# Performance work log

Measured on AMD Instinct MI355X. Metric: run time of the kernel, lower is better.

The kernel has to match this reference:

```python
import jax, jax.numpy as jnp
import numpy as np

B, T, OUT, H = 4096, 128, 64, 200


def lstm_cell(x_t, h, c, Wih, Whh, b):
    # PyTorch gate order: input, forget, cell(g), output
    gates = x_t @ Wih.T + h @ Whh.T + b  # [B, 4H]
    i, f, g, o = jnp.split(gates, 4, axis=-1)
    c = jax.nn.sigmoid(f) * c + jax.nn.sigmoid(i) * jnp.tanh(g)
    h = jax.nn.sigmoid(o) * jnp.tanh(c)
    return h, c


def lstm_layer(xs, Wih, Whh, b, h0, c0):
    # xs: [T, B, D] -> ys: [T, B, H], final (h, c)
    def step(carry, x_t):
        h, c = lstm_cell(x_t, carry[0], carry[1], Wih, Whh, b)
        return (h, c), h
    (h, c), ys = jax.lax.scan(step, (h0, c0), xs)
    return ys, h, c


def setup_inputs() -> dict:
    key = jax.random.key(0)
    ks = jax.random.split(key, 16)
    s = 0.05
    inp = {"x": jax.random.normal(ks[0], (B, T), dtype=jnp.float32)}
    # encoder layer 0 (input size 1), layer 1 (input size H)
    inp["enc_Wih0"] = jax.random.normal(ks[1], (4 * H, 1), jnp.float32) * s
    inp["enc_Whh0"] = jax.random.normal(ks[2], (4 * H, H), jnp.float32) * s
    inp["enc_b0"] = jnp.zeros((4 * H,), jnp.float32)
    inp["enc_Wih1"] = jax.random.normal(ks[3], (4 * H, H), jnp.float32) * s
    inp["enc_Whh1"] = jax.random.normal(ks[4], (4 * H, H), jnp.float32) * s
    inp["enc_b1"] = jnp.zeros((4 * H,), jnp.float32)
    # decoder layers
    inp["dec_Wih0"] = jax.random.normal(ks[5], (4 * H, 1), jnp.float32) * s
    inp["dec_Whh0"] = jax.random.normal(ks[6], (4 * H, H), jnp.float32) * s
    inp["dec_b0"] = jnp.zeros((4 * H,), jnp.float32)
    inp["dec_Wih1"] = jax.random.normal(ks[7], (4 * H, H), jnp.float32) * s
    inp["dec_Whh1"] = jax.random.normal(ks[8], (4 * H, H), jnp.float32) * s
    inp["dec_b1"] = jnp.zeros((4 * H,), jnp.float32)
    # output linear: hid -> 1
    inp["lin_W"] = jax.random.normal(ks[9], (1, H), jnp.float32) * s
    inp["lin_b"] = jnp.zeros((1,), jnp.float32)
    return inp


def reference(x, enc_Wih0, enc_Whh0, enc_b0, enc_Wih1, enc_Whh1, enc_b1,
              dec_Wih0, dec_Whh0, dec_b0, dec_Wih1, dec_Whh1, dec_b1,
              lin_W, lin_b):
    b = x.shape[0]
    z = jnp.zeros((b, H), x.dtype)
    xs = x.T[:, :, None]  # [T, B, 1]
    # encoder (2-layer LSTM; dropout is a no-op in eval mode)
    ys1, h1, c1 = lstm_layer(xs, enc_Wih0, enc_Whh0, enc_b0, z, z)
    _, h2, c2 = lstm_layer(ys1, enc_Wih1, enc_Whh1, enc_b1, z, z)

    def dec_step(carry, _):
        h1, c1, h2, c2, inp = carry
        h1, c1 = lstm_cell(inp, h1, c1, dec_Wih0, dec_Whh0, dec_b0)
        h2, c2 = lstm_cell(h1, h2, c2, dec_Wih1, dec_Whh1, dec_b1)
        pred = h2 @ lin_W.T + lin_b  # [B, 1]
        return (h1, c1, h2, c2, pred), pred[:, 0]

    carry0 = (h1, c1, h2, c2, x[:, -1:])
    _, preds = jax.lax.scan(dec_step, carry0, None, length=OUT)  # [OUT, B]
    return preds.T  # [B, OUT]
```

## Files before the change

### kernel.cpp

```cpp
#include <hip/hip_runtime.h>
#include <math.h>

#define HID   200
#define G4    800
#define BB    16
#define NTH   512
#define SEQT  128
#define NOUT  64
#define WKP   224
#define AST   232
#define GST   802
#define MATU  (G4 * WKP)

typedef __attribute__((ext_vector_type(8))) short short8;
typedef __attribute__((ext_vector_type(4))) float f32x4;
typedef unsigned short ushort_t;

__device__ __forceinline__ unsigned short bf16_rne(float v) {
    unsigned int u = __float_as_uint(v);
    u = u + 0x7FFFu + ((u >> 16) & 1u);
    return (unsigned short)(u >> 16);
}

__global__ void prep_weights(const float* __restrict__ s0, const float* __restrict__ s1,
                             const float* __restrict__ s2, const float* __restrict__ s3,
                             const float* __restrict__ s4, const float* __restrict__ s5,
                             unsigned short* __restrict__ ws) {
    const float* src;
    int m = blockIdx.y;
    switch (m) {
        case 0: src = s0; break;
        case 1: src = s1; break;
        case 2: src = s2; break;
        case 3: src = s3; break;
        case 4: src = s4; break;
        default: src = s5; break;
    }
    int i = blockIdx.x * blockDim.x + threadIdx.x;
    int n = i / WKP;
    int k = i - n * WKP;
    float v = (k < HID) ? src[n * HID + k] : 0.0f;
    unsigned short hi = bf16_rne(v);
    float rem = v - __uint_as_float(((unsigned int)hi) << 16);
    unsigned short lo = bf16_rne(rem);
    ws[(size_t)(2 * m) * MATU + i]     = hi;
    ws[(size_t)(2 * m + 1) * MATU + i] = lo;
}

__device__ __forceinline__ short8 ldA(const unsigned short* h, int lane, int c) {
    return *(const short8*)(h + (lane & 15) * AST + c * 32 + ((lane >> 4) << 3));
}

template<int NT>
__device__ __forceinline__ void mm_pass(const unsigned short* __restrict__ Whi,
                                        const unsigned short* __restrict__ Wlo,
                                        const unsigned short* hhi, const unsigned short* hlo,
                                        int lane, int tile0, f32x4* acc) {
    short8 ahi[7], alo[7];
#pragma unroll
    for (int c = 0; c < 7; ++c) { ahi[c] = ldA(hhi, lane, c); alo[c] = ldA(hlo, lane, c); }
    const int ko   = (lane >> 4) << 3;
    const int nrow = lane & 15;
#pragma unroll
    for (int t = 0; t < NT; ++t) {
        const unsigned short* wp = Whi + (size_t)((tile0 + t) * 16 + nrow) * WKP + ko;
        const unsigned short* wq = Wlo + (size_t)((tile0 + t) * 16 + nrow) * WKP + ko;
#pragma unroll
        for (int c = 0; c < 7; ++c) {
            short8 bhi = *(const short8*)(wp + c * 32);
            short8 blo = *(const short8*)(wq + c * 32);
            acc[t] = __builtin_amdgcn_mfma_f32_16x16x32_bf16(ahi[c], bhi, acc[t], 0, 0, 0);
            acc[t] = __builtin_amdgcn_mfma_f32_16x16x32_bf16(ahi[c], blo, acc[t], 0, 0, 0);
            acc[t] = __builtin_amdgcn_mfma_f32_16x16x32_bf16(alo[c], bhi, acc[t], 0, 0, 0);
        }
    }
}

template<int NT>
__device__ __forceinline__ void cell_mm_s(float* gates,
        const unsigned short* Whi, const unsigned short* Wlo,
        const unsigned short* hhi, const unsigned short* hlo,
        const float* __restrict__ bias, const float* __restrict__ wih,
        const float* xcol, int lane, int tile0) {
    f32x4 acc[NT];
    const int nrow = lane & 15;
    const int bg   = (lane >> 4) << 2;
#pragma unroll
    for (int t = 0; t < NT; ++t) {
        int n = (tile0 + t) * 16 + nrow;
        float bj = bias[n], wj = wih[n];
#pragma unroll
        for (int r = 0; r < 4; ++r) acc[t][r] = fmaf(xcol[bg + r], wj, bj);
    }
    mm_pass<NT>(Whi, Wlo, hhi, hlo, lane, tile0, acc);
#pragma unroll
    for (int t = 0; t < NT; ++t) {
        int n = (tile0 + t) * 16 + nrow;
#pragma unroll
        for (int r = 0; r < 4; ++r) gates[(bg + r) * GST + n] = acc[t][r];
    }
}

template<int NT>
__device__ __forceinline__ void cell_mm_v(float* gates,
        const unsigned short* Wihhi, const unsigned short* Wihlo,
        const unsigned short* Whhhi, const unsigned short* Whhlo,
        const unsigned short* hxhi, const unsigned short* hxlo,
        const unsigned short* hhhi, const unsigned short* hhlo,
        const float* __restrict__ bias, int lane, int tile0) {
    f32x4 acc[NT];
    const int nrow = lane & 15;
    const int bg   = (lane >> 4) << 2;
#pragma unroll
    for (int t = 0; t < NT; ++t) {
        float bj = bias[(tile0 + t) * 16 + nrow];
        acc[t] = (f32x4){bj, bj, bj, bj};
    }
    mm_pass<NT>(Wihhi, Wihlo, hxhi, hxlo, lane, tile0, acc);
    mm_pass<NT>(Whhhi, Whhlo, hhhi, hhlo, lane, tile0, acc);
#pragma unroll
    for (int t = 0; t < NT; ++t) {
        int n = (tile0 + t) * 16 + nrow;
#pragma unroll
        for (int r = 0; r < 4; ++r) gates[(bg + r) * GST + n] = acc[t][r];
    }
}

__device__ __forceinline__ float fsig(float v) {
    return __builtin_amdgcn_rcpf(1.0f + __expf(-v));
}
__device__ __forceinline__ float ftanh(float v) {
    return 1.0f - 2.0f * __builtin_amdgcn_rcpf(__expf(2.0f * v) + 1.0f);
}

__device__ __forceinline__ void cell_ew(const float* gates,
                                        unsigned short* hhi, unsigned short* hlo,
                                        float* cv, int tid) {
#pragma unroll
    for (int r = 0; r < 7; ++r) {
        int i = tid + r * NTH;
        if (i < BB * HID) {
            int b = i / HID;
            int m = i - b * HID;
            const float* g = gates + b * GST;
            float gi = g[m], gf = g[HID + m], gg = g[2 * HID + m], go = g[3 * HID + m];
            float cp = cv[r];
            float cn = fsig(gf) * cp + fsig(gi) * ftanh(gg);
            cv[r] = cn;
            float h = fsig(go) * ftanh(cn);
            unsigned short hb = bf16_rne(h);
            float rem = h - __uint_as_float(((unsigned int)hb) << 16);
            unsigned short lb = bf16_rne(rem);
            hhi[b * AST + m] = hb;
            hlo[b * AST + m] = lb;
        }
    }
}

__global__ __launch_bounds__(NTH, 2)
void lstm_mfma(const float* __restrict__ x,
               const float* __restrict__ eWih0, const float* __restrict__ eB0,
               const float* __restrict__ eB1,
               const float* __restrict__ dWih0, const float* __restrict__ dB0,
               const float* __restrict__ dB1,
               const float* __restrict__ linW, const float* __restrict__ linb,
               const unsigned short* __restrict__ wst,
               float* __restrict__ out) {
    extern __shared__ char smraw[];
    float* gates = (float*)smraw;
    float* xsT   = gates + BB * GST;
    float* linWs = xsT + SEQT * BB;
    float* predb = linWs + HID;
    float* part  = predb + BB;
    unsigned short* h1hi = (unsigned short*)(part + BB * 4);
    unsigned short* h1lo = h1hi + BB * AST;
    unsigned short* h2hi = h1lo + BB * AST;
    unsigned short* h2lo = h2hi + BB * AST;

    const unsigned short* eWhh0hi = wst;
    const unsigned short* eWhh0lo = wst + MATU;
    const unsigned short* eWih1hi = wst + 2 * MATU;
    const unsigned short* eWih1lo = wst + 3 * MATU;
    const unsigned short* eWhh1hi = wst + 4 * MATU;
    const unsigned short* eWhh1lo = wst + 5 * MATU;
    const unsigned short* dWhh0hi = wst + 6 * MATU;
    const unsigned short* dWhh0lo = wst + 7 * MATU;
    const unsigned short* dWih1hi = wst + 8 * MATU;
    const unsigned short* dWih1lo = wst + 9 * MATU;
    const unsigned short* dWhh1hi = wst + 10 * MATU;
    const unsigned short* dWhh1lo = wst + 11 * MATU;

    const int tid  = threadIdx.x;
    const int lane = tid & 63;
    const int w    = tid >> 6;
    const int b0g  = blockIdx.x * BB;
    const int tile0 = (w < 2) ? 7 * w : 14 + 6 * (w - 2);

    for (int i = tid; i < BB * AST; i += NTH) {
        h1hi[i] = 0; h1lo[i] = 0; h2hi[i] = 0; h2lo[i] = 0;
    }
    for (int i = tid; i < BB * SEQT; i += NTH) {
        int b = i >> 7, t = i & (SEQT - 1);
        xsT[t * BB + b] = x[(size_t)(b0g + b) * SEQT + t];
    }
    for (int i = tid; i < HID; i += NTH) linWs[i] = linW[i];
    float c1v[7], c2v[7];
#pragma unroll
    for (int r = 0; r < 7; ++r) { c1v[r] = 0.0f; c2v[r] = 0.0f; }
    __syncthreads();

    for (int t = 0; t < SEQT; ++t) {
        const float* xcol = xsT + t * BB;
        if (w < 2) cell_mm_s<7>(gates, eWhh0hi, eWhh0lo, h1hi, h1lo, eB0, eWih0, xcol, lane, tile0);
        else       cell_mm_s<6>(gates, eWhh0hi, eWhh0lo, h1hi, h1lo, eB0, eWih0, xcol, lane, tile0);
        __syncthreads();
        cell_ew(gates, h1hi, h1lo, c1v, tid);
        __syncthreads();
        if (w < 2) cell_mm_v<7>(gates, eWih1hi, eWih1lo, eWhh1hi, eWhh1lo, h1hi, h1lo, h2hi, h2lo, eB1, lane, tile0);
        else       cell_mm_v<6>(gates, eWih1hi, eWih1lo, eWhh1hi, eWhh1lo, h1hi, h1lo, h2hi, h2lo, eB1, lane, tile0);
        __syncthreads();
        cell_ew(gates, h2hi, h2lo, c2v, tid);
        __syncthreads();
    }

    if (tid < BB) predb[tid] = xsT[(SEQT - 1) * BB + tid];
    __syncthreads();

    for (int s = 0; s < NOUT; ++s) {
        if (w < 2) cell_mm_s<7>(gates, dWhh0hi, dWhh0lo, h1hi, h1lo, dB0, dWih0, predb, lane, tile0);
        else       cell_mm_s<6>(gates, dWhh0hi, dWhh0lo, h1hi, h1lo, dB0, dWih0, predb, lane, tile0);
        __syncthreads();
        cell_ew(gates, h1hi, h1lo, c1v, tid);
        __syncthreads();
        if (w < 2) cell_mm_v<7>(gates, dWih1hi, dWih1lo, dWhh1hi, dWhh1lo, h1hi, h1lo, h2hi, h2lo, dB1, lane, tile0);
        else       cell_mm_v<6>(gates, dWih1hi, dWih1lo, dWhh1hi, dWhh1lo, h1hi, h1lo, h2hi, h2lo, dB1, lane, tile0);
        __syncthreads();
        cell_ew(gates, h2hi, h2lo, c2v, tid);
        __syncthreads();
        if (tid < 64) {
            int b = tid >> 2, q = tid & 3;
            const unsigned short* ph = h2hi + b * AST + q * 50;
            const unsigned short* pl = h2lo + b * AST + q * 50;
            const float* lw = linWs + q * 50;
            float p = 0.0f;
#pragma unroll 10
            for (int k = 0; k < 50; ++k) {
                float hv = __uint_as_float(((unsigned int)ph[k]) << 16)
                         + __uint_as_float(((unsigned int)pl[k]) << 16);
                p = fmaf(hv, lw[k], p);
            }
            part[tid] = p;
        }
        __syncthreads();
        if (tid < BB) {
            float p = part[tid * 4] + part[tid * 4 + 1] + part[tid * 4 + 2] + part[tid * 4 + 3]
                    + linb[0];
            predb[tid] = p;
            out[(size_t)(b0g + tid) * NOUT + s] = p;
        }
        __syncthreads();
    }
}

extern "C" void kernel_launch(void* const* d_in, const int* in_sizes, int n_in,
                              void* d_out, int out_size, void* d_ws, size_t ws_size,
                              hipStream_t stream) {
    const float* x     = (const float*)d_in[0];
    const float* eWih0 = (const float*)d_in[1];
    const float* eWhh0 = (const float*)d_in[2];
    const float* eB0   = (const float*)d_in[3];
    const float* eWih1 = (const float*)d_in[4];
    const float* eWhh1 = (const float*)d_in[5];
    const float* eB1   = (const float*)d_in[6];
    const float* dWih0 = (const float*)d_in[7];
    const float* dWhh0 = (const float*)d_in[8];
    const float* dB0   = (const float*)d_in[9];
    const float* dWih1 = (const float*)d_in[10];
    const float* dWhh1 = (const float*)d_in[11];
    const float* dB1   = (const float*)d_in[12];
    const float* linW  = (const float*)d_in[13];
    const float* linb  = (const float*)d_in[14];
    unsigned short* ws = (unsigned short*)d_ws;
    float* out = (float*)d_out;

    prep_weights<<<dim3(MATU / 256, 6), 256, 0, stream>>>(
        eWhh0, eWih1, eWhh1, dWhh0, dWih1, dWhh1, ws);

    size_t smem = (size_t)(BB * GST + SEQT * BB + HID + BB + BB * 4) * sizeof(float)
                + (size_t)(4 * BB * AST) * sizeof(unsigned short);
    (void)hipFuncSetAttribute((const void*)lstm_mfma,
                              hipFuncAttributeMaxDynamicSharedMemorySize, 160 * 1024);
    lstm_mfma<<<dim3(4096 / BB), dim3(NTH), smem, stream>>>(
        x, eWih0, eB0, eB1, dWih0, dB0, dB1, linW, linb, ws, out);
}
```

Before: 10.33 ms.

## Split hidden units across blocks with LDS-resident weights and grid barriers

Adds a new persistent kernel that partitions the hidden dimension across 32 blocks per batch group of 512 rows, so each block keeps its slice of the weights resident in LDS in hi/lo bf16 form. Hidden states are exchanged through global memory, staged into LDS with direct global-to-LDS loads, and synchronised per group with atomic spin barriers. This removes the repeated streaming of all weights from global/L2 at every timestep that the old batch-tiled kernel paid. In exchange it adds global-memory traffic for hidden states and barrier latency on every step, and it relies on all 256 blocks being co-resident. The old path is kept as a fallback when the workspace is too small.

```diff
diff --git a/kernel.cpp b/kernel.cpp
--- a/kernel.cpp
+++ b/kernel.cpp
@@ -1,31 +1,357 @@
 #include <hip/hip_runtime.h>
 #include <math.h>
 
-#define HID   200
-#define G4    800
+typedef unsigned short u16;
+typedef unsigned int   u32;
+typedef __attribute__((ext_vector_type(8))) short short8;
+typedef __attribute__((ext_vector_type(4))) float f32x4;
+
+#define HID  200
+#define G4   800
+#define SEQT 128
+#define NOUT 64
+#define NTH  512
+#define WKP  224
+
+__device__ __forceinline__ float fsig(float v) {
+    return __builtin_amdgcn_rcpf(1.0f + __expf(-v));
+}
+__device__ __forceinline__ float ftanh(float v) {
+    return 1.0f - 2.0f * __builtin_amdgcn_rcpf(__expf(2.0f * v) + 1.0f);
+}
+__device__ __forceinline__ u16 bf16_rne(float v) {
+    u32 u = __float_as_uint(v);
+    u = u + 0x7FFFu + ((u >> 16) & 1u);
+    return (u16)(u >> 16);
+}
+
+#define HST   200
+#define WSTR  232
+#define GSTR  34
+#define PLN2  ((size_t)4096*HST)
+
+#define WS_PRED 0
+#define WS_BAR  16384
+#define WS_H    18432
+#define WS_TAIL (WS_H + 8*(int)(PLN2*2))
+#define WS_FAST (WS_TAIL + 256)
+
+#define L_A2   (6*32*WSTR*2)
+#define L_G2   (L_A2 + 4*14336)
+#define L_TOT2 (L_G2 + 64*GSTR*4)
+
+__global__ void init_fast(char* __restrict__ ws) {
+    size_t n = WS_FAST / 4;
+    u32* p = (u32*)ws;
+    size_t stride = (size_t)gridDim.x * blockDim.x;
+    for (size_t i = (size_t)blockIdx.x * blockDim.x + threadIdx.x; i < n; i += stride)
+        p[i] = 0u;
+}
+
+__device__ __forceinline__ void gbar(u32* barr, int g, unsigned& mygen) {
+    __syncthreads();
+    if (threadIdx.x == 0) {
+        u32* cnt = barr + g * 64;
+        u32* gen = barr + g * 64 + 32;
+        unsigned target = mygen + 1;
+        __threadfence();
+        unsigned old = __hip_atomic_fetch_add(cnt, 1u, __ATOMIC_ACQ_REL, __HIP_MEMORY_SCOPE_AGENT);
+        if (old == 31u) {
+            __hip_atomic_store(cnt, 0u, __ATOMIC_RELAXED, __HIP_MEMORY_SCOPE_AGENT);
+            __hip_atomic_fetch_add(gen, 1u, __ATOMIC_RELEASE, __HIP_MEMORY_SCOPE_AGENT);
+        } else {
+            while (__hip_atomic_load(gen, __ATOMIC_ACQUIRE, __HIP_MEMORY_SCOPE_AGENT) < target)
+                __builtin_amdgcn_s_sleep(4);
+        }
+        __threadfence();
+    }
+    __syncthreads();
+    mygen += 1;
+}
+
+__device__ __forceinline__ void load_weights_f32(u16* Wl,
+        const float* __restrict__ M0, const float* __restrict__ M1,
+        const float* __restrict__ M2,
+        int NRr, int cnt, int csh, int m0, int tid) {
+    int tot = 3 * NRr * WKP;
+    for (int idx = tid; idx < tot; idx += NTH) {
+        int k   = idx % WKP;
+        int rem = idx / WKP;
+        int rr  = rem % NRr;
+        int mi  = rem / NRr;
+        const float* M = (mi == 0) ? M0 : ((mi == 1) ? M1 : M2);
+        int q = rr >> csh, i = rr & (cnt - 1);
+        int n = 200 * q + m0 + i;
+        float v = (k < HID) ? M[n * HID + k] : 0.0f;
+        u16 hi = bf16_rne(v);
+        float r2 = v - __uint_as_float(((u32)hi) << 16);
+        u16 lo = bf16_rne(r2);
+        Wl[(2 * mi)     * (32 * WSTR) + rr * WSTR + k] = hi;
+        Wl[(2 * mi + 1) * (32 * WSTR) + rr * WSTR + k] = lo;
+    }
+}
+
+__device__ __forceinline__ void stageA2(char* Ab, const u16* __restrict__ Ahi,
+                                        const u16* __restrict__ Alo, int brow0, int w, int lane) {
+    const u16* src = (w & 1) ? Alo : Ahi;
+    char* lb = Ab + (w >> 1) * 14336 + (w & 1) * 7168;
+    const u16* g0 = src + (size_t)(brow0 + ((w >> 1) << 4) + (lane & 15)) * HST + ((lane >> 4) << 3);
+#pragma unroll
+    for (int c = 0; c < 7; ++c) {
+        __builtin_amdgcn_global_load_lds(
+            (const __attribute__((address_space(1))) u32*)(g0 + c * 32),
+            (__attribute__((address_space(3))) u32*)(lb + c * 1024),
+            16, 0, 0);
+    }
+}
+
+__device__ __forceinline__ void loadB2(const u16* Wl, int mp, int ntw, int lane, short8* B) {
+    const u16* b0 = Wl + mp * (32 * WSTR) + (ntw * 16 + (lane & 15)) * WSTR + ((lane >> 4) << 3);
+#pragma unroll
+    for (int c = 0; c < 7; ++c) B[c] = *(const short8*)(b0 + c * 32);
+}
+
+__device__ __forceinline__ void mmpass2(const char* Ab, const short8* Bh, const short8* Bl,
+                                        f32x4& aa, f32x4& ab, int w, int lane) {
+    const char* a0 = Ab + (w >> 1) * 14336;
+#pragma unroll
+    for (int c = 0; c < 7; ++c) {
+        short8 ahi = *(const short8*)(a0 + c * 1024 + lane * 16);
+        short8 alo = *(const short8*)(a0 + 7168 + c * 1024 + lane * 16);
+        if (c & 1) {
+            ab = __builtin_amdgcn_mfma_f32_16x16x32_bf16(ahi, Bh[c], ab, 0, 0, 0);
+            ab = __builtin_amdgcn_mfma_f32_16x16x32_bf16(ahi, Bl[c], ab, 0, 0, 0);
+            ab = __builtin_amdgcn_mfma_f32_16x16x32_bf16(alo, Bh[c], ab, 0, 0, 0);
+        } else {
+            aa = __builtin_amdgcn_mfma_f32_16x16x32_bf16(ahi, Bh[c], aa, 0, 0, 0);
+            aa = __builtin_amdgcn_mfma_f32_16x16x32_bf16(ahi, Bl[c], aa, 0, 0, 0);
+            aa = __builtin_amdgcn_mfma_f32_16x16x32_bf16(alo, Bh[c], aa, 0, 0, 0);
+        }
+    }
+}
+
+__device__ __forceinline__ void gwrite2(float* gb, f32x4 aa, f32x4 ab, int w, int lane) {
+    int row0 = ((w >> 1) << 4) + ((lane >> 4) << 2);
+    int col  = (w & 1) * 16 + (lane & 15);
+#pragma unroll
+    for (int j = 0; j < 4; ++j) gb[(row0 + j) * GSTR + col] = aa[j] + ab[j];
+}
+
+__device__ __forceinline__ void ew2(const float* gb, float& creg,
+                                    u16* __restrict__ Ohi, u16* __restrict__ Olo,
+                                    int babs0, int tid, int heavy, int cnt, int csh, int m0) {
+    if (heavy || tid < 256) {
+        int b_loc = tid >> csh, i = tid & (cnt - 1);
+        const float* gg = gb + b_loc * GSTR;
+        float vi = gg[i], vf = gg[cnt + i], vg = gg[2 * cnt + i], vo = gg[3 * cnt + i];
+        float cn = fsig(vf) * creg + fsig(vi) * ftanh(vg);
+        creg = cn;
+        float h = fsig(vo) * ftanh(cn);
+        u16 hv = bf16_rne(h);
+        float r2 = h - __uint_as_float(((u32)hv) << 16);
+        u16 lv = bf16_rne(r2);
+        size_t o = (size_t)(babs0 + b_loc) * HST + m0 + i;
+        Ohi[o] = hv;
+        Olo[o] = lv;
+    }
+}
+
+__device__ __forceinline__ void cell_l1f(
+    u16* Wl, char* Ab, float* gb,
+    const u16* Ahi, const u16* Alo, u16* Ohi, u16* Olo,
+    const float* __restrict__ psrc, int pstr, int poff,
+    const float* __restrict__ wihv, const float* __restrict__ biasv, float* c1,
+    int tid, int lane, int w, int ntw, int NT, int heavy, int cnt, int csh, int m0, int b0g)
+{
+    short8 Bh[7], Bl[7];
+    float bj = 0.f, wj = 0.f;
+    if (ntw < NT) {
+        loadB2(Wl, 0, ntw, lane, Bh);
+        loadB2(Wl, 1, ntw, lane, Bl);
+        int nl = ntw * 16 + (lane & 15);
+        int q = nl >> csh, i = nl & (cnt - 1);
+        int n = 200 * q + m0 + i;
+        bj = biasv[n];
+        wj = wihv[n];
+    }
+#pragma unroll
+    for (int ch = 0; ch < 8; ++ch) {
+        stageA2(Ab, Ahi, Alo, b0g + ch * 64, w, lane);
+        if (ch > 0) ew2(gb, c1[ch - 1], Ohi, Olo, b0g + (ch - 1) * 64, tid, heavy, cnt, csh, m0);
+        asm volatile("s_waitcnt vmcnt(0)" ::: "memory");
+        __syncthreads();
+        if (ntw < NT) {
+            int br0 = b0g + ch * 64 + ((w >> 1) << 4) + ((lane >> 4) << 2);
+            f32x4 aa, ab = (f32x4){0.f, 0.f, 0.f, 0.f};
+#pragma unroll
+            for (int j = 0; j < 4; ++j) aa[j] = fmaf(psrc[(size_t)(br0 + j) * pstr + poff], wj, bj);
+            mmpass2(Ab, Bh, Bl, aa, ab, w, lane);
+            gwrite2(gb, aa, ab, w, lane);
+        }
+        __syncthreads();
+    }
+    ew2(gb, c1[7], Ohi, Olo, b0g + 7 * 64, tid, heavy, cnt, csh, m0);
+}
+
+__device__ __forceinline__ void cell_l2f(
+    u16* Wl, char* Ab, float* gb,
+    const u16* A1hi, const u16* A1lo, const u16* A2hi, const u16* A2lo,
+    u16* Ohi, u16* Olo,
+    const float* __restrict__ biasv, float* c2,
+    int tid, int lane, int w, int ntw, int NT, int heavy, int cnt, int csh, int m0, int b0g)
+{
+    short8 B1h[7], B1l[7], B2h[7], B2l[7];
+    float bj = 0.f;
+    if (ntw < NT) {
+        loadB2(Wl, 2, ntw, lane, B1h);
+        loadB2(Wl, 3, ntw, lane, B1l);
+        loadB2(Wl, 4, ntw, lane, B2h);
+        loadB2(Wl, 5, ntw, lane, B2l);
+        int nl = ntw * 16 + (lane & 15);
+        int q = nl >> csh, i = nl & (cnt - 1);
+        bj = biasv[200 * q + m0 + i];
+    }
+#pragma unroll
+    for (int ch = 0; ch < 8; ++ch) {
+        stageA2(Ab, A1hi, A1lo, b0g + ch * 64, w, lane);
+        if (ch > 0) ew2(gb, c2[ch - 1], Ohi, Olo, b0g + (ch - 1) * 64, tid, heavy, cnt, csh, m0);
+        asm volatile("s_waitcnt vmcnt(0)" ::: "memory");
+        __syncthreads();
+        f32x4 aa = (f32x4){bj, bj, bj, bj}, ab = (f32x4){0.f, 0.f, 0.f, 0.f};
+        if (ntw < NT) mmpass2(Ab, B1h, B1l, aa, ab, w, lane);
+        __syncthreads();
+        stageA2(Ab, A2hi, A2lo, b0g + ch * 64, w, lane);
+        asm volatile("s_waitcnt vmcnt(0)" ::: "memory");
+        __syncthreads();
+        if (ntw < NT) {
+            mmpass2(Ab, B2h, B2l, aa, ab, w, lane);
+            gwrite2(gb, aa, ab, w, lane);
+        }
+        __syncthreads();
+    }
+    ew2(gb, c2[7], Ohi, Olo, b0g + 7 * 64, tid, heavy, cnt, csh, m0);
+}
+
+__device__ __forceinline__ void predp2(
+    float* ps, const u16* __restrict__ H2hi, const u16* __restrict__ H2lo,
+    const float* __restrict__ linW, const float* __restrict__ linb,
+    float* __restrict__ predG, float* __restrict__ out,
+    int sdec, int b0g, int s, int tid)
+{
+    int bi = tid >> 5, kk = tid & 31;
+    float part = 0.f;
+    size_t rb = (size_t)(b0g + s * 16 + bi) * HST;
+#pragma unroll
+    for (int j = 0; j < 7; ++j) {
+        int k = kk + 32 * j;
+        if (k < HID) {
+            float hv = __uint_as_float(((u32)H2hi[rb + k]) << 16)
+                     + __uint_as_float(((u32)H2lo[rb + k]) << 16);
+            part = fmaf(hv, linW[k], part);
+        }
+    }
+    ps[bi * 33 + kk] = part;
+    __syncthreads();
+    if (tid < 16) {
+        float p = linb[0];
+#pragma unroll
+        for (int k2 = 0; k2 < 32; ++k2) p += ps[tid * 33 + k2];
+        predG[b0g + s * 16 + tid] = p;
+        out[(size_t)(b0g + s * 16 + tid) * NOUT + sdec] = p;
+    }
+    __syncthreads();
+}
+
+__global__ __launch_bounds__(NTH, 2)
+void lstm_fast(const float* __restrict__ x,
+               const float* __restrict__ eWih0, const float* __restrict__ eWhh0,
+               const float* __restrict__ eB0,
+               const float* __restrict__ eWih1, const float* __restrict__ eWhh1,
+               const float* __restrict__ eB1,
+               const float* __restrict__ dWih0, const float* __restrict__ dWhh0,
+               const float* __restrict__ dB0,
+               const float* __restrict__ dWih1, const float* __restrict__ dWhh1,
+               const float* __restrict__ dB1,
+               const float* __restrict__ linW, const float* __restrict__ linb,
+               u16* hb, float* predG, u32* barr, float* __restrict__ out)
+{
+    extern __shared__ char sm[];
+    u16*  Wl = (u16*)sm;
+    char* Ab = sm + L_A2;
+    float* gb = (float*)(sm + L_G2);
+
+    const int tid = threadIdx.x, lane = tid & 63, w = tid >> 6;
+    const int g = blockIdx.x & 7, s = blockIdx.x >> 3;
+    const int heavy = (s < 18) ? 1 : 0;
+    const int cnt = heavy ? 8 : 4;
+    const int csh = heavy ? 3 : 2;
+    const int m0  = heavy ? 8 * s : 144 + 4 * (s - 18);
+    const int NT  = cnt >> 2;
+    const int ntw = w & 1;
+    const int b0g = g * 512;
+    unsigned mygen = 0;
+
+    load_weights_f32(Wl, eWhh0, eWih1, eWhh1, 4 * cnt, cnt, csh, m0, tid);
+    __syncthreads();
+
+    float c1[8], c2[8];
+#pragma unroll
+    for (int i = 0; i < 8; ++i) { c1[i] = 0.f; c2[i] = 0.f; }
+    int p1 = 0, p2 = 0;
+
+    for (int t = 0; t < SEQT; ++t) {
+        cell_l1f(Wl, Ab, gb,
+                 hb + (size_t)(2 * p1) * PLN2, hb + (size_t)(2 * p1 + 1) * PLN2,
+                 hb + (size_t)(2 * (p1 ^ 1)) * PLN2, hb + (size_t)(2 * (p1 ^ 1) + 1) * PLN2,
+                 x, SEQT, t, eWih0, eB0, c1,
+                 tid, lane, w, ntw, NT, heavy, cnt, csh, m0, b0g);
+        p1 ^= 1;
+        gbar(barr, g, mygen);
+        cell_l2f(Wl, Ab, gb,
+                 hb + (size_t)(2 * p1) * PLN2, hb + (size_t)(2 * p1 + 1) * PLN2,
+                 hb + (size_t)(4 + 2 * p2) * PLN2, hb + (size_t)(4 + 2 * p2 + 1) * PLN2,
+                 hb + (size_t)(4 + 2 * (p2 ^ 1)) * PLN2, hb + (size_t)(4 + 2 * (p2 ^ 1) + 1) * PLN2,
+                 eB1, c2, tid, lane, w, ntw, NT, heavy, cnt, csh, m0, b0g);
+        p2 ^= 1;
+    }
+
+    __syncthreads();
+    load_weights_f32(Wl, dWhh0, dWih1, dWhh1, 4 * cnt, cnt, csh, m0, tid);
+    __syncthreads();
+
+    for (int sd = 0; sd < NOUT; ++sd) {
+        const float* psrc = (sd == 0) ? x : predG;
+        int pstr = (sd == 0) ? SEQT : 1;
+        int poff = (sd == 0) ? (SEQT - 1) : 0;
+        cell_l1f(Wl, Ab, gb,
+                 hb + (size_t)(2 * p1) * PLN2, hb + (size_t)(2 * p1 + 1) * PLN2,
+                 hb + (size_t)(2 * (p1 ^ 1)) * PLN2, hb + (size_t)(2 * (p1 ^ 1) + 1) * PLN2,
+                 psrc, pstr, poff, dWih0, dB0, c1,
+                 tid, lane, w, ntw, NT, heavy, cnt, csh, m0, b0g);
+        p1 ^= 1;
+        gbar(barr, g, mygen);
+        cell_l2f(Wl, Ab, gb,
+                 hb + (size_t)(2 * p1) * PLN2, hb + (size_t)(2 * p1 + 1) * PLN2,
+                 hb + (size_t)(4 + 2 * p2) * PLN2, hb + (size_t)(4 + 2 * p2 + 1) * PLN2,
+                 hb + (size_t)(4 + 2 * (p2 ^ 1)) * PLN2, hb + (size_t)(4 + 2 * (p2 ^ 1) + 1) * PLN2,
+                 dB1, c2, tid, lane, w, ntw, NT, heavy, cnt, csh, m0, b0g);
+        p2 ^= 1;
+        gbar(barr, g, mygen);
+        predp2(gb, hb + (size_t)(4 + 2 * p2) * PLN2, hb + (size_t)(4 + 2 * p2 + 1) * PLN2,
+               linW, linb, predG, out, sd, b0g, s, tid);
+        gbar(barr, g, mygen);
+    }
+}
+
 #define BB    16
-#define NTH   512
-#define SEQT  128
-#define NOUT  64
-#define WKP   224
 #define AST   232
 #define GST   802
 #define MATU  (G4 * WKP)
 
-typedef __attribute__((ext_vector_type(8))) short short8;
-typedef __attribute__((ext_vector_type(4))) float f32x4;
-typedef unsigned short ushort_t;
-
-__device__ __forceinline__ unsigned short bf16_rne(float v) {
-    unsigned int u = __float_as_uint(v);
-    u = u + 0x7FFFu + ((u >> 16) & 1u);
-    return (unsigned short)(u >> 16);
-}
-
 __global__ void prep_weights(const float* __restrict__ s0, const float* __restrict__ s1,
                              const float* __restrict__ s2, const float* __restrict__ s3,
                              const float* __restrict__ s4, const float* __restrict__ s5,
-                             unsigned short* __restrict__ ws) {
+                             u16* __restrict__ ws) {
     const float* src;
     int m = blockIdx.y;
     switch (m) {
@@ -40,31 +366,31 @@
     int n = i / WKP;
     int k = i - n * WKP;
     float v = (k < HID) ? src[n * HID + k] : 0.0f;
-    unsigned short hi = bf16_rne(v);
-    float rem = v - __uint_as_float(((unsigned int)hi) << 16);
-    unsigned short lo = bf16_rne(rem);
+    u16 hi = bf16_rne(v);
+    float rem = v - __uint_as_float(((u32)hi) << 16);
+    u16 lo = bf16_rne(rem);
     ws[(size_t)(2 * m) * MATU + i]     = hi;
     ws[(size_t)(2 * m + 1) * MATU + i] = lo;
 }
 
-__device__ __forceinline__ short8 ldA(const unsigned short* h, int lane, int c) {
+__device__ __forceinline__ short8 ldA_r3(const u16* h, int lane, int c) {
     return *(const short8*)(h + (lane & 15) * AST + c * 32 + ((lane >> 4) << 3));
 }
 
 template<int NT>
-__device__ __forceinline__ void mm_pass(const unsigned short* __restrict__ Whi,
-                                        const unsigned short* __restrict__ Wlo,
-                                        const unsigned short* hhi, const unsigned short* hlo,
-                                        int lane, int tile0, f32x4* acc) {
+__device__ __forceinline__ void mm_pass_r3(const u16* __restrict__ Whi,
+                                           const u16* __restrict__ Wlo,
+                                           const u16* hhi, const u16* hlo,
+                                           int lane, int tile0, f32x4* acc) {
     short8 ahi[7], alo[7];
 #pragma unroll
-    for (int c = 0; c < 7; ++c) { ahi[c] = ldA(hhi, lane, c); alo[c] = ldA(hlo, lane, c); }
+    for (int c = 0; c < 7; ++c) { ahi[c] = ldA_r3(hhi, lane, c); alo[c] = ldA_r3(hlo, lane, c); }
     const int ko   = (lane >> 4) << 3;
     const int nrow = lane & 15;
 #pragma unroll
     for (int t = 0; t < NT; ++t) {
-        const unsigned short* wp = Whi + (size_t)((tile0 + t) * 16 + nrow) * WKP + ko;
-        const unsigned short* wq = Wlo + (size_t)((tile0 + t) * 16 + nrow) * WKP + ko;
+        const u16* wp = Whi + (size_t)((tile0 + t) * 16 + nrow) * WKP + ko;
+        const u16* wq = Wlo + (size_t)((tile0 + t) * 16 + nrow) * WKP + ko;
 #pragma unroll
         for (int c = 0; c < 7; ++c) {
             short8 bhi = *(const short8*)(wp + c * 32);
@@ -77,9 +403,8 @@
 }
 
 template<int NT>
-__device__ __forceinline__ void cell_mm_s(float* gates,
-        const unsigned short* Whi, const unsigned short* Wlo,
-        const unsigned short* hhi, const unsigned short* hlo,
+__device__ __forceinline__ void cell_mm_s_r3(float* gates,
+        const u16* Whi, const u16* Wlo, const u16* hhi, const u16* hlo,
         const float* __restrict__ bias, const float* __restrict__ wih,
         const float* xcol, int lane, int tile0) {
     f32x4 acc[NT];
@@ -92,7 +417,7 @@
 #pragma unroll
         for (int r = 0; r < 4; ++r) acc[t][r] = fmaf(xcol[bg + r], wj, bj);
     }
-    mm_pass<NT>(Whi, Wlo, hhi, hlo, lane, tile0, acc);
+    mm_pass_r3<NT>(Whi, Wlo, hhi, hlo, lane, tile0, acc);
 #pragma unroll
     for (int t = 0; t < NT; ++t) {
         int n = (tile0 + t) * 16 + nrow;
@@ -102,11 +427,9 @@
 }
 
 template<int NT>
-__device__ __forceinline__ void cell_mm_v(float* gates,
-        const unsigned short* Wihhi, const unsigned short* Wihlo,
-        const unsigned short* Whhhi, const unsigned short* Whhlo,
-        const unsigned short* hxhi, const unsigned short* hxlo,
-        const unsigned short* hhhi, const unsigned short* hhlo,
+__device__ __forceinline__ void cell_mm_v_r3(float* gates,
+        const u16* Wihhi, const u16* Wihlo, const u16* Whhhi, const u16* Whhlo,
+        const u16* hxhi, const u16* hxlo, const u16* hhhi, const u16* hhlo,
         const float* __restrict__ bias, int lane, int tile0) {
     f32x4 acc[NT];
     const int nrow = lane & 15;
@@ -116,8 +439,8 @@
         float bj = bias[(tile0 + t) * 16 + nrow];
         acc[t] = (f32x4){bj, bj, bj, bj};
     }
-    mm_pass<NT>(Wihhi, Wihlo, hxhi, hxlo, lane, tile0, acc);
-    mm_pass<NT>(Whhhi, Whhlo, hhhi, hhlo, lane, tile0, acc);
+    mm_pass_r3<NT>(Wihhi, Wihlo, hxhi, hxlo, lane, tile0, acc);
+    mm_pass_r3<NT>(Whhhi, Whhlo, hhhi, hhlo, lane, tile0, acc);
 #pragma unroll
     for (int t = 0; t < NT; ++t) {
         int n = (tile0 + t) * 16 + nrow;
@@ -126,16 +449,8 @@
     }
 }
 
-__device__ __forceinline__ float fsig(float v) {
-    return __builtin_amdgcn_rcpf(1.0f + __expf(-v));
-}
-__device__ __forceinline__ float ftanh(float v) {
-    return 1.0f - 2.0f * __builtin_amdgcn_rcpf(__expf(2.0f * v) + 1.0f);
-}
-
-__device__ __forceinline__ void cell_ew(const float* gates,
-                                        unsigned short* hhi, unsigned short* hlo,
-                                        float* cv, int tid) {
+__device__ __forceinline__ void cell_ew_r3(const float* gates,
+                                           u16* hhi, u16* hlo, float* cv, int tid) {
 #pragma unroll
     for (int r = 0; r < 7; ++r) {
         int i = tid + r * NTH;
@@ -148,9 +463,9 @@
             float cn = fsig(gf) * cp + fsig(gi) * ftanh(gg);
             cv[r] = cn;
             float h = fsig(go) * ftanh(cn);
-            unsigned short hb = bf16_rne(h);
-            float rem = h - __uint_as_float(((unsigned int)hb) << 16);
-            unsigned short lb = bf16_rne(rem);
+            u16 hb = bf16_rne(h);
+            float rem = h - __uint_as_float(((u32)hb) << 16);
+            u16 lb = bf16_rne(rem);
             hhi[b * AST + m] = hb;
             hlo[b * AST + m] = lb;
         }
@@ -164,7 +479,7 @@
                const float* __restrict__ dWih0, const float* __restrict__ dB0,
                const float* __restrict__ dB1,
                const float* __restrict__ linW, const float* __restrict__ linb,
-               const unsigned short* __restrict__ wst,
+               const u16* __restrict__ wst,
                float* __restrict__ out) {
     extern __shared__ char smraw[];
     float* gates = (float*)smraw;
@@ -172,23 +487,23 @@
     float* linWs = xsT + SEQT * BB;
     float* predb = linWs + HID;
     float* part  = predb + BB;
-    unsigned short* h1hi = (unsigned short*)(part + BB * 4);
-    unsigned short* h1lo = h1hi + BB * AST;
-    unsigned short* h2hi = h1lo + BB * AST;
-    unsigned short* h2lo = h2hi + BB * AST;
-
-    const unsigned short* eWhh0hi = wst;
-    const unsigned short* eWhh0lo = wst + MATU;
-    const unsigned short* eWih1hi = wst + 2 * MATU;
-    const unsigned short* eWih1lo = wst + 3 * MATU;
-    const unsigned short* eWhh1hi = wst + 4 * MATU;
-    const unsigned short* eWhh1lo = wst + 5 * MATU;
-    const unsigned short* dWhh0hi = wst + 6 * MATU;
-    const unsigned short* dWhh0lo = wst + 7 * MATU;
-    const unsigned short* dWih1hi = wst + 8 * MATU;
-    const unsigned short* dWih1lo = wst + 9 * MATU;
-    const unsigned short* dWhh1hi = wst + 10 * MATU;
-    const unsigned short* dWhh1lo = wst + 11 * MATU;
+    u16* h1hi = (u16*)(part + BB * 4);
+    u16* h1lo = h1hi + BB * AST;
+    u16* h2hi = h1lo + BB * AST;
+    u16* h2lo = h2hi + BB * AST;
+
+    const u16* eWhh0hi = wst;
+    const u16* eWhh0lo = wst + MATU;
+    const u16* eWih1hi = wst + 2 * MATU;
+    const u16* eWih1lo = wst + 3 * MATU;
+    const u16* eWhh1hi = wst + 4 * MATU;
+    const u16* eWhh1lo = wst + 5 * MATU;
+    const u16* dWhh0hi = wst + 6 * MATU;
+    const u16* dWhh0lo = wst + 7 * MATU;
+    const u16* dWih1hi = wst + 8 * MATU;
+    const u16* dWih1lo = wst + 9 * MATU;
+    const u16* dWhh1hi = wst + 10 * MATU;
+    const u16* dWhh1lo = wst + 11 * MATU;
 
     const int tid  = threadIdx.x;
     const int lane = tid & 63;
@@ -211,15 +526,15 @@
 
     for (int t = 0; t < SEQT; ++t) {
         const float* xcol = xsT + t * BB;
-        if (w < 2) cell_mm_s<7>(gates, eWhh0hi, eWhh0lo, h1hi, h1lo, eB0, eWih0, xcol, lane, tile0);
-        else       cell_mm_s<6>(gates, eWhh0hi, eWhh0lo, h1hi, h1lo, eB0, eWih0, xcol, lane, tile0);
-        __syncthreads();
-        cell_ew(gates, h1hi, h1lo, c1v, tid);
-        __syncthreads();
-        if (w < 2) cell_mm_v<7>(gates, eWih1hi, eWih1lo, eWhh1hi, eWhh1lo, h1hi, h1lo, h2hi, h2lo, eB1, lane, tile0);
-        else       cell_mm_v<6>(gates, eWih1hi, eWih1lo, eWhh1hi, eWhh1lo, h1hi, h1lo, h2hi, h2lo, eB1, lane, tile0);
-        __syncthreads();
-        cell_ew(gates, h2hi, h2lo, c2v, tid);
+        if (w < 2) cell_mm_s_r3<7>(gates, eWhh0hi, eWhh0lo, h1hi, h1lo, eB0, eWih0, xcol, lane, tile0);
+        else       cell_mm_s_r3<6>(gates, eWhh0hi, eWhh0lo, h1hi, h1lo, eB0, eWih0, xcol, lane, tile0);
+        __syncthreads();
+        cell_ew_r3(gates, h1hi, h1lo, c1v, tid);
+        __syncthreads();
+        if (w < 2) cell_mm_v_r3<7>(gates, eWih1hi, eWih1lo, eWhh1hi, eWhh1lo, h1hi, h1lo, h2hi, h2lo, eB1, lane, tile0);
+        else       cell_mm_v_r3<6>(gates, eWih1hi, eWih1lo, eWhh1hi, eWhh1lo, h1hi, h1lo, h2hi, h2lo, eB1, lane, tile0);
+        __syncthreads();
+        cell_ew_r3(gates, h2hi, h2lo, c2v, tid);
         __syncthreads();
     }
 
@@ -227,26 +542,26 @@
     __syncthreads();
 
     for (int s = 0; s < NOUT; ++s) {
-        if (w < 2) cell_mm_s<7>(gates, dWhh0hi, dWhh0lo, h1hi, h1lo, dB0, dWih0, predb, lane, tile0);
-        else       cell_mm_s<6>(gates, dWhh0hi, dWhh0lo, h1hi, h1lo, dB0, dWih0, predb, lane, tile0);
-        __syncthreads();
-        cell_ew(gates, h1hi, h1lo, c1v, tid);
-        __syncthreads();
-        if (w < 2) cell_mm_v<7>(gates, dWih1hi, dWih1lo, dWhh1hi, dWhh1lo, h1hi, h1lo, h2hi, h2lo, dB1, lane, tile0);
-        else       cell_mm_v<6>(gates, dWih1hi, dWih1lo, dWhh1hi, dWhh1lo, h1hi, h1lo, h2hi, h2lo, dB1, lane, tile0);
-        __syncthreads();
-        cell_ew(gates, h2hi, h2lo, c2v, tid);
+        if (w < 2) cell_mm_s_r3<7>(gates, dWhh0hi, dWhh0lo, h1hi, h1lo, dB0, dWih0, predb, lane, tile0);
+        else       cell_mm_s_r3<6>(gates, dWhh0hi, dWhh0lo, h1hi, h1lo, dB0, dWih0, predb, lane, tile0);
+        __syncthreads();
+        cell_ew_r3(gates, h1hi, h1lo, c1v, tid);
+        __syncthreads();
+        if (w < 2) cell_mm_v_r3<7>(gates, dWih1hi, dWih1lo, dWhh1hi, dWhh1lo, h1hi, h1lo, h2hi, h2lo, dB1, lane, tile0);
+        else       cell_mm_v_r3<6>(gates, dWih1hi, dWih1lo, dWhh1hi, dWhh1lo, h1hi, h1lo, h2hi, h2lo, dB1, lane, tile0);
+        __syncthreads();
+        cell_ew_r3(gates, h2hi, h2lo, c2v, tid);
         __syncthreads();
         if (tid < 64) {
             int b = tid >> 2, q = tid & 3;
-            const unsigned short* ph = h2hi + b * AST + q * 50;
-            const unsigned short* pl = h2lo + b * AST + q * 50;
+            const u16* ph = h2hi + b * AST + q * 50;
+            const u16* pl = h2lo + b * AST + q * 50;
             const float* lw = linWs + q * 50;
             float p = 0.0f;
 #pragma unroll 10
             for (int k = 0; k < 50; ++k) {
-                float hv = __uint_as_float(((unsigned int)ph[k]) << 16)
-                         + __uint_as_float(((unsigned int)pl[k]) << 16);
+                float hv = __uint_as_float(((u32)ph[k]) << 16)
+                         + __uint_as_float(((u32)pl[k]) << 16);
                 p = fmaf(hv, lw[k], p);
             }
             part[tid] = p;
@@ -280,16 +595,30 @@
     const float* dB1   = (const float*)d_in[12];
     const float* linW  = (const float*)d_in[13];
     const float* linb  = (const float*)d_in[14];
-    unsigned short* ws = (unsigned short*)d_ws;
     float* out = (float*)d_out;
-
-    prep_weights<<<dim3(MATU / 256, 6), 256, 0, stream>>>(
-        eWhh0, eWih1, eWhh1, dWhh0, dWih1, dWhh1, ws);
-
-    size_t smem = (size_t)(BB * GST + SEQT * BB + HID + BB + BB * 4) * sizeof(float)
-                + (size_t)(4 * BB * AST) * sizeof(unsigned short);
-    (void)hipFuncSetAttribute((const void*)lstm_mfma,
-                              hipFuncAttributeMaxDynamicSharedMemorySize, 160 * 1024);
-    lstm_mfma<<<dim3(4096 / BB), dim3(NTH), smem, stream>>>(
-        x, eWih0, eB0, eB1, dWih0, dB0, dB1, linW, linb, ws, out);
-}
+    char* ws = (char*)d_ws;
+
+    if (ws_size >= (size_t)WS_FAST) {
+        float* predG = (float*)(ws + WS_PRED);
+        u32*   barr  = (u32*)(ws + WS_BAR);
+        u16*   hbp   = (u16*)(ws + WS_H);
+
+        init_fast<<<dim3(1024), dim3(256), 0, stream>>>(ws);
+        (void)hipFuncSetAttribute((const void*)lstm_fast,
+                                  hipFuncAttributeMaxDynamicSharedMemorySize, L_TOT2);
+        lstm_fast<<<dim3(256), dim3(NTH), L_TOT2, stream>>>(
+            x, eWih0, eWhh0, eB0, eWih1, eWhh1, eB1,
+            dWih0, dWhh0, dB0, dWih1, dWhh1, dB1,
+            linW, linb, hbp, predG, barr, out);
+    } else {
+        u16* wst = (u16*)ws;
+        prep_weights<<<dim3(MATU / 256, 6), 256, 0, stream>>>(
+            eWhh0, eWih1, eWhh1, dWhh0, dWih1, dWhh1, wst);
+        size_t smem = (size_t)(BB * GST + SEQT * BB + HID + BB + BB * 4) * sizeof(float)
+                    + (size_t)(4 * BB * AST) * sizeof(u16);
+        (void)hipFuncSetAttribute((const void*)lstm_mfma,
+                                  hipFuncAttributeMaxDynamicSharedMemorySize, 160 * 1024);
+        lstm_mfma<<<dim3(4096 / BB), dim3(NTH), smem, stream>>>(
+            x, eWih0, eB0, eB1, dWih0, dB0, dB1, linW, linb, wst, out);
+    }
+}
```

Result: slower. 16.04 ms (+55.3%).
